# Performance work log

Measured on AMD Instinct MI355X. Metric: run time of the kernel, lower is better.

Reference implementation:

```python
import jax, jax.numpy as jnp
import numpy as np

B, S, D = 2, 2048, 1024
H, DH = 16, 64
DM = 4096
NEG = 1e10


def setup_inputs() -> dict:
    key = jax.random.key(0)
    ks = jax.random.split(key, 8)
    sc = 1.0 / np.sqrt(D)
    return {
        "x": jax.random.normal(ks[0], (B, S, D), jnp.float32),
        "W_Q": jax.random.normal(ks[1], (H, DH, D), jnp.float32) * sc,
        "W_K": jax.random.normal(ks[2], (H, DH, D), jnp.float32) * sc,
        "W_V": jax.random.normal(ks[3], (H, DH, D), jnp.float32) * sc,
        "W_O": jax.random.normal(ks[4], (D, H * DH), jnp.float32) * sc,
        "W_in": jax.random.normal(ks[5], (DM, D), jnp.float32) * sc,
        "b_in": jnp.zeros((DM,), jnp.float32),
        "W_out": jax.random.normal(ks[6], (D, DM), jnp.float32) * sc,
        "b_out": jnp.zeros((D,), jnp.float32),
    }


def reference(x, W_Q, W_K, W_V, W_O, W_in, b_in, W_out, b_out):
    b, s, d = x.shape
    d_head = W_Q.shape[1]
    # --- Attention (faithful to original einsum/mask formulation) ---
    q = jnp.einsum('ihd,bpd->biph', W_Q, x)
    k = jnp.einsum('ihd,bpd->biph', W_K, x)
    v = jnp.einsum('ihd,bpd->biph', W_V, x)
    scores = jnp.einsum('biph,biqh->biqp', k, q)  # [b,i,q,p]
    # original: t.tril(scores) - 1e10 * (1 - triu(ones)) ; mask buffer is triu
    triu = jnp.triu(jnp.ones((s, s), x.dtype))
    masked = jnp.tril(scores) - NEG * (1.0 - triu)
    attn = jax.nn.softmax(masked / np.sqrt(d_head), axis=-1)
    z = jnp.einsum('biph,biqp->biqh', v, attn)          # [b,i,q,h]
    z_flat = z.transpose(0, 2, 1, 3).reshape(b, s, -1)   # b q (i h)
    attn_out = jnp.einsum('df,bqf->bqd', W_O, z_flat)
    # --- Block residual structure (as written: x = attn(x); x = x + x) ---
    mid = attn_out + attn_out
    # --- MLP ---
    pre = jnp.einsum('md,bpd->bpm', W_in, mid) + b_in
    h = jax.nn.relu(pre)
    mlp_out = jnp.einsum('dm,bpm->bpd', W_out, h) + b_out
    return mid + mlp_out
```

## Files before the change

kernel.cpp:

```cpp
#include <hip/hip_runtime.h>
#include <hip/hip_bf16.h>
#include <stdint.h>

typedef unsigned short ushort_t;
typedef __attribute__((ext_vector_type(8))) short short8;
typedef __attribute__((ext_vector_type(4))) float floatx4;

#define DEV __device__ __forceinline__

DEV ushort_t f2b(float f) {
  uint32_t x = __float_as_uint(f);
  uint32_t r = (x + 0x7FFFu + ((x >> 16) & 1u)) >> 16;
  return (ushort_t)r;
}
DEV float b2f(ushort_t u) { return __uint_as_float(((uint32_t)u) << 16); }

DEV void async16(const ushort_t* g, ushort_t* l) {
  __builtin_amdgcn_global_load_lds(
      (const __attribute__((address_space(1))) void*)g,
      (__attribute__((address_space(3))) void*)l, 16, 0, 0);
}

struct Cvt7 {
  const float* src[7];
  ushort_t* dst[7];
  float scale[7];
  unsigned start[8];
};
__global__ void cvt_all(Cvt7 a) {
  unsigned idx = blockIdx.x * blockDim.x + threadIdx.x;
  if (idx >= a.start[7]) return;
  int seg = 0;
#pragma unroll
  for (int j = 1; j < 7; j++) seg += (idx >= a.start[j]) ? 1 : 0;
  unsigned off = idx - a.start[seg];
  float sc = a.scale[seg];
  float4 v = ((const float4*)a.src[seg])[off];
  ((ushort4*)a.dst[seg])[off] =
      make_ushort4(f2b(v.x * sc), f2b(v.y * sc), f2b(v.z * sc), f2b(v.w * sc));
}

template <int MODE, int MT, int SWZ>
__launch_bounds__(256)
__global__ void gemm_bt(const ushort_t* __restrict__ A, const ushort_t* __restrict__ Bm,
                        int M, int N, int Kd, int ldk,
                        ushort_t* __restrict__ outB, float* __restrict__ outF,
                        const float* __restrict__ bias) {
  constexpr int TM = 32 * MT;
  __shared__ alignas(16) ushort_t As[TM * 64];
  __shared__ alignas(16) ushort_t Bs[128 * 64];
  const int tid = threadIdx.x;
  const int wave = tid >> 6, lane = tid & 63;
  const int wm = wave >> 1, wn = wave & 1;

  int bx, by;
  if constexpr (SWZ == 1) {
    const int f = blockIdx.x + gridDim.x * blockIdx.y;
    by = (f & 7) + 8 * (f / (8 * gridDim.x));
    bx = (f >> 3) % gridDim.x;
  } else if constexpr (SWZ == 2) {
    const int x = blockIdx.x, y = blockIdx.y;
    bx = 2 * (x & 3) + (y & 1);
    by = (y >> 1) + 32 * (x >> 2);
  } else {
    bx = blockIdx.x; by = blockIdx.y;
  }
  const int m0 = by * TM, n0 = bx * 128;
  const int kz = blockIdx.z * Kd;

  floatx4 acc[MT][4];
#pragma unroll
  for (int i = 0; i < MT; i++)
#pragma unroll
    for (int j = 0; j < 4; j++) acc[i][j] = (floatx4){0.f, 0.f, 0.f, 0.f};

  const int r8 = lane >> 3;
  const int scol = (((lane & 7) ^ (r8 & 7)) * 8);
  const ushort_t* gA = A + (size_t)(m0 + wave * (TM / 4) + r8) * ldk + kz + scol;
  const ushort_t* gB = Bm + (size_t)(n0 + wave * 32 + r8) * ldk + kz + scol;
  ushort_t* lA = As + wave * (TM / 4) * 64;
  ushort_t* lB = Bs + wave * 2048;

  const int fr = lane & 15, fq = lane >> 4;
  const int sw = fr & 7;
  const ushort_t* rdA = As + (wm * 16 * MT + fr) * 64;
  const ushort_t* rdB = Bs + (wn * 64 + fr) * 64;

  for (int k0 = 0; k0 < Kd; k0 += 64) {
#pragma unroll
    for (int j = 0; j < MT; j++) async16(gA + (size_t)j * 8 * ldk, lA + j * 512);
#pragma unroll
    for (int j = 0; j < 4; j++) async16(gB + (size_t)j * 8 * ldk, lB + j * 512);
    gA += 64; gB += 64;
    __syncthreads();
#pragma unroll
    for (int h = 0; h < 2; h++) {
      const int co = ((h * 4 + fq) ^ sw) * 8;
      short8 af[MT], bfv[4];
#pragma unroll
      for (int mt = 0; mt < MT; mt++) af[mt] = *(const short8*)(rdA + mt * 16 * 64 + co);
#pragma unroll
      for (int nt = 0; nt < 4; nt++) bfv[nt] = *(const short8*)(rdB + nt * 16 * 64 + co);
#pragma unroll
      for (int mt = 0; mt < MT; mt++)
#pragma unroll
        for (int nt = 0; nt < 4; nt++)
          acc[mt][nt] = __builtin_amdgcn_mfma_f32_16x16x32_bf16(af[mt], bfv[nt], acc[mt][nt], 0, 0, 0);
    }
    __syncthreads();
  }

  const int crow = m0 + wm * 16 * MT + (lane >> 4) * 4;
  const int ccol = n0 + wn * 64 + (lane & 15);
  const size_t zoff = (size_t)blockIdx.z * M * N;
#pragma unroll
  for (int mt = 0; mt < MT; mt++)
#pragma unroll
    for (int nt = 0; nt < 4; nt++) {
      floatx4 a = acc[mt][nt];
#pragma unroll
      for (int r = 0; r < 4; r++) {
        const int gm = crow + mt * 16 + r;
        const int gn = ccol + nt * 16;
        const size_t idx = (size_t)gm * N + gn;
        float v = a[r];
        if constexpr (MODE == 0) {
          outB[idx] = f2b(v);
        } else if constexpr (MODE == 1) {
          outB[idx] = f2b(v);
          outF[idx] = v + bias[gn];
        } else if constexpr (MODE == 2) {
          float t = v + bias[gn];
          outB[idx] = f2b(t > 0.f ? t : 0.f);
        } else {
          outF[zoff + idx] = v;
        }
      }
    }
}

template <int MODE>
__launch_bounds__(512, 2)
__global__ void gemm256(const ushort_t* __restrict__ A, const ushort_t* __restrict__ Bm,
                        int M, int N, int Kd, int ldk,
                        ushort_t* __restrict__ outB, float* __restrict__ outF,
                        const float* __restrict__ bias) {
  __shared__ alignas(16) ushort_t As[4][256 * 32];
  __shared__ alignas(16) ushort_t Bs[4][256 * 32];
  const int tid = threadIdx.x;
  const int lane = tid & 63;
  const int wave = tid >> 6;
  const int wm = wave >> 2, wn = wave & 3;

  const int gy = gridDim.y;
  int f = blockIdx.x + gridDim.x * blockIdx.y;
  {
    const int nwg = gridDim.x * gy;
    const int q = nwg >> 3, rr = nwg & 7;
    const int xcd = f & 7, ix = f >> 3;
    f = (xcd < rr ? xcd * (q + 1) : rr * (q + 1) + (xcd - rr) * q) + ix;
  }
  const int bx = f / gy, by = f - gy * bx;
  const int m0 = by * 256, n0 = bx * 256;
  const size_t kz = (size_t)blockIdx.z * Kd;

  floatx4 acc[8][4];
#pragma unroll
  for (int i = 0; i < 8; i++)
#pragma unroll
    for (int j = 0; j < 4; j++) acc[i][j] = (floatx4){0.f, 0.f, 0.f, 0.f};

  const int rloc = tid >> 2, cch = tid & 3;
  const int gcol = ((cch ^ ((rloc >> 1) & 3)) * 8);
  const ushort_t* gA = A + (size_t)(m0 + rloc) * ldk + kz + gcol;
  const ushort_t* gB = Bm + (size_t)(n0 + rloc) * ldk + kz + gcol;
  const int lofs = rloc * 32 + cch * 8;

#define STGA32(bufi, kofs)                                              \
  {                                                                     \
    async16(gA + (kofs), &As[bufi][lofs]);                              \
    async16(gA + (size_t)128 * ldk + (kofs), &As[bufi][4096 + lofs]);   \
  }
#define STGB32(bufi, kofs)                                              \
  {                                                                     \
    async16(gB + (kofs), &Bs[bufi][lofs]);                              \
    async16(gB + (size_t)128 * ldk + (kofs), &Bs[bufi][4096 + lofs]);   \
  }

  const int NT = Kd >> 5;
  STGA32(0, 0) STGB32(0, 0)
  if (NT > 1) { STGA32(1, 32) STGB32(1, 32) }
  if (NT > 2) { STGA32(2, 64) STGB32(2, 64) }
  if (NT > 2) asm volatile("s_waitcnt vmcnt(8)" ::: "memory");
  else if (NT > 1) asm volatile("s_waitcnt vmcnt(4)" ::: "memory");
  else asm volatile("s_waitcnt vmcnt(0)" ::: "memory");
  __builtin_amdgcn_s_barrier();

  const int fr = lane & 15, fq = lane >> 4;
  const int co = ((fq ^ ((fr >> 1) & 3)) * 8);
  const int aoff = (wm * 128 + fr) * 32 + co;
  const int boff = (wn * 64 + fr) * 32 + co;

  for (int kt = 0; kt < NT; ++kt) {
    const int cb = kt & 3;
    const int pb = (kt + 3) & 3;
    const int kof = (kt + 3) * 32;
    const bool sp = (kt + 3) < NT;
    const ushort_t* Ab = As[cb];
    const ushort_t* Bb = Bs[cb];
    short8 av[4], bv[4];

#pragma unroll
    for (int i = 0; i < 4; i++) av[i] = *(const short8*)(Ab + aoff + i * 512);
#pragma unroll
    for (int j = 0; j < 4; j++) bv[j] = *(const short8*)(Bb + boff + j * 512);
    if (sp) STGA32(pb, kof)
    __builtin_amdgcn_s_barrier();
    asm volatile("s_waitcnt lgkmcnt(0)" ::: "memory");
    __builtin_amdgcn_s_setprio(1);
#pragma unroll
    for (int i = 0; i < 4; i++)
#pragma unroll
      for (int j = 0; j < 4; j++)
        acc[i][j] = __builtin_amdgcn_mfma_f32_16x16x32_bf16(av[i], bv[j], acc[i][j], 0, 0, 0);
    __builtin_amdgcn_s_setprio(0);
    __builtin_amdgcn_s_barrier();

#pragma unroll
    for (int i = 0; i < 4; i++) av[i] = *(const short8*)(Ab + aoff + 2048 + i * 512);
    if (sp) STGB32(pb, kof)
    __builtin_amdgcn_s_barrier();
    asm volatile("s_waitcnt lgkmcnt(0)" ::: "memory");
    __builtin_amdgcn_s_setprio(1);
#pragma unroll
    for (int i = 0; i < 4; i++)
#pragma unroll
      for (int j = 0; j < 4; j++)
        acc[4 + i][j] = __builtin_amdgcn_mfma_f32_16x16x32_bf16(av[i], bv[j], acc[4 + i][j], 0, 0, 0);
    __builtin_amdgcn_s_setprio(0);
    if (kt + 3 < NT) asm volatile("s_waitcnt vmcnt(8)" ::: "memory");
    else if (kt + 2 < NT) asm volatile("s_waitcnt vmcnt(4)" ::: "memory");
    else asm volatile("s_waitcnt vmcnt(0)" ::: "memory");
    __builtin_amdgcn_s_barrier();
  }
#undef STGA32
#undef STGB32

  const int crow = m0 + wm * 128 + (lane >> 4) * 4;
  const int ccol = n0 + wn * 64 + (lane & 15);
  const size_t zoff = (size_t)blockIdx.z * ((size_t)M * (size_t)N);
#pragma unroll
  for (int mt = 0; mt < 8; mt++)
#pragma unroll
    for (int nt = 0; nt < 4; nt++) {
      floatx4 a = acc[mt][nt];
#pragma unroll
      for (int r = 0; r < 4; r++) {
        const int gm = crow + mt * 16 + r;
        const int gn = ccol + nt * 16;
        const size_t idx = (size_t)gm * N + gn;
        if constexpr (MODE == 0) {
          outB[idx] = f2b(a[r]);
        } else if constexpr (MODE == 2) {
          float t = a[r] + bias[gn];
          outB[idx] = f2b(t > 0.f ? t : 0.f);
        } else {
          outF[zoff + idx] = a[r];
        }
      }
    }
}

__launch_bounds__(256)
__global__ void reduce4(const float4* __restrict__ P, float4* __restrict__ out, int n4) {
  int i = blockIdx.x * blockDim.x + threadIdx.x;
  int st = gridDim.x * blockDim.x;
  for (; i < n4; i += st) {
    float4 a = out[i];
    float4 p0 = P[i], p1 = P[i + 1048576], p2 = P[i + 2097152], p3 = P[i + 3145728];
    a.x += (p0.x + p1.x) + (p2.x + p3.x);
    a.y += (p0.y + p1.y) + (p2.y + p3.y);
    a.z += (p0.z + p1.z) + (p2.z + p3.z);
    a.w += (p0.w + p1.w) + (p2.w + p3.w);
    out[i] = a;
  }
}

__launch_bounds__(256)
__global__ void attn1(const ushort_t* __restrict__ qkv,
                      float* __restrict__ eG, float* __restrict__ psumG) {
  const int c = blockIdx.x & 63;
  const int i = (blockIdx.x >> 6) & 15;
  const int b = blockIdx.x >> 10;
  const int t = threadIdx.x, wave = t >> 6, h = t & 63;
  const size_t rowbase = (size_t)b * 2048 * 3072;
  float vacc = 0.f;
#pragma unroll
  for (int r = 0; r < 8; r++) {
    const int s = c * 32 + wave * 8 + r;
    const size_t rb = rowbase + (size_t)s * 3072 + i * 64 + h;
    float q = b2f(qkv[rb]);
    float k = b2f(qkv[rb + 1024]);
    float v = b2f(qkv[rb + 2048]);
    float d = q * k;
#pragma unroll
    for (int off = 32; off > 0; off >>= 1) d += __shfl_xor(d, off, 64);
    if (h == 0) eG[((size_t)(b * 16 + i)) * 2048 + s] = __expf(d * 0.125f);
    vacc += v;
  }
  __shared__ float vs[4][64];
  vs[wave][h] = vacc;
  __syncthreads();
  if (t < 64)
    psumG[(((size_t)(b * 16 + i)) * 64 + c) * 64 + t] =
        vs[0][t] + vs[1][t] + vs[2][t] + vs[3][t];
}

__launch_bounds__(256)
__global__ void attn2(const ushort_t* __restrict__ qkv,
                      const float* __restrict__ eG, const float* __restrict__ psumG,
                      ushort_t* __restrict__ Z) {
  const int wave = threadIdx.x >> 6, h = threadIdx.x & 63;
  const int c = (blockIdx.x & 15) * 4 + wave;
  const int i = (blockIdx.x >> 4) & 15;
  const int b = blockIdx.x >> 8;
  const size_t rowbase = (size_t)b * 2048 * 3072;
  const size_t pbase = ((size_t)(b * 16 + i)) * 64;
  float run = 0.f;
#pragma unroll 8
  for (int cc = c + 1; cc < 64; cc++) run += psumG[(pbase + cc) * 64 + h];
  const size_t ebase = ((size_t)(b * 16 + i)) * 2048;
  for (int t4 = 1; t4 >= 0; t4--) {
    float vv[16], ee[16];
#pragma unroll
    for (int j = 0; j < 16; j++) {
      const int s = c * 32 + t4 * 16 + j;
      vv[j] = b2f(qkv[rowbase + (size_t)s * 3072 + 2048 + i * 64 + h]);
      ee[j] = eG[ebase + s];
    }
#pragma unroll
    for (int j = 15; j >= 0; j--) {
      const int s = c * 32 + t4 * 16 + j;
      float z = (ee[j] * vv[j] + run) / (ee[j] + (float)(2047 - s));
      Z[((size_t)b * 2048 + s) * 1024 + i * 64 + h] = f2b(z);
      run += vv[j];
    }
  }
}

extern "C" void kernel_launch(void* const* d_in, const int* in_sizes, int n_in,
                              void* d_out, int out_size, void* d_ws, size_t ws_size,
                              hipStream_t stream) {
  const float* x     = (const float*)d_in[0];
  const float* W_Q   = (const float*)d_in[1];
  const float* W_K   = (const float*)d_in[2];
  const float* W_V   = (const float*)d_in[3];
  const float* W_O   = (const float*)d_in[4];
  const float* W_in  = (const float*)d_in[5];
  const float* b_in  = (const float*)d_in[6];
  const float* W_out = (const float*)d_in[7];
  const float* b_out = (const float*)d_in[8];
  float* out = (float*)d_out;

  char* base = (char*)d_ws;
  const size_t MB = 1048576;
  ushort_t* Xb    = (ushort_t*)(base + 0 * MB);
  ushort_t* Wqkv  = (ushort_t*)(base + 8 * MB);
  ushort_t* WOb   = (ushort_t*)(base + 14 * MB);
  ushort_t* Z     = (ushort_t*)(base + 16 * MB);
  ushort_t* QKV   = (ushort_t*)(base + 24 * MB);
  ushort_t* midb  = (ushort_t*)(base + 48 * MB);
  ushort_t* Winb  = (ushort_t*)(base + 56 * MB);
  ushort_t* Woutb = (ushort_t*)(base + 64 * MB);
  ushort_t* Hb    = (ushort_t*)(base + 72 * MB);
  float*    P     = (float*)(base + 0 * MB);
  float*    psumG = (float*)(base + 72 * MB);
  float*    eG    = (float*)(base + 72 * MB + 524288);

  Cvt7 ca;
  ca.src[0] = x;     ca.dst[0] = Xb;               ca.scale[0] = 1.f;
  ca.src[1] = W_Q;   ca.dst[1] = Wqkv;             ca.scale[1] = 1.f;
  ca.src[2] = W_K;   ca.dst[2] = Wqkv + 1048576;   ca.scale[2] = 1.f;
  ca.src[3] = W_V;   ca.dst[3] = Wqkv + 2097152;   ca.scale[3] = 1.f;
  ca.src[4] = W_O;   ca.dst[4] = WOb;              ca.scale[4] = 2.f;
  ca.src[5] = W_in;  ca.dst[5] = Winb;             ca.scale[5] = 1.f;
  ca.src[6] = W_out; ca.dst[6] = Woutb;            ca.scale[6] = 1.f;
  unsigned n4s[7] = {1048576, 262144, 262144, 262144, 262144, 1048576, 1048576};
  unsigned acc4 = 0;
  for (int j = 0; j < 7; j++) { ca.start[j] = acc4; acc4 += n4s[j]; }
  ca.start[7] = acc4;
  cvt_all<<<dim3((acc4 + 255) / 256), dim3(256), 0, stream>>>(ca);

  gemm256<0><<<dim3(12, 16), 512, 0, stream>>>(Xb, Wqkv, 4096, 3072, 1024, 1024,
                                               QKV, nullptr, nullptr);
  attn1<<<dim3(2048), 256, 0, stream>>>(QKV, eG, psumG);
  attn2<<<dim3(512), 256, 0, stream>>>(QKV, eG, psumG, Z);
  gemm_bt<1, 2, 1><<<dim3(8, 64), 256, 0, stream>>>(Z, WOb, 4096, 1024, 1024, 1024,
                                                    midb, out, b_out);
  gemm256<2><<<dim3(16, 16), 512, 0, stream>>>(midb, Winb, 4096, 4096, 1024, 1024,
                                               Hb, nullptr, b_in);
  gemm256<3><<<dim3(4, 16, 4), 512, 0, stream>>>(Hb, Woutb, 4096, 1024, 1024, 4096,
                                                 nullptr, P, nullptr);
  reduce4<<<dim3(1024), 256, 0, stream>>>((const float4*)P, (float4*)out, 1048576);
}
```

Before: 290.3 us.

## Software-pipeline LDS fragment loads with MFMA in GEMM main loop

Restructures the GEMM K-loop so LDS reads for the next half-tile and the next k-step's A/B fragments are issued before or during the current MFMA block, using double-buffered A registers and interleaving B reloads between MFMA columns. The explicit lgkmcnt waits and one of the two barriers per half are removed, and sched_barrier plus compiler fences pin the ordering. The prologue drops the NT>1/NT>2 guards, assuming K is at least 96. The aim is to hide LDS latency behind matrix instructions and cut barrier stalls, at the cost of more live vector registers and a possible occupancy drop or spills.

```diff
diff --git a/kernel.cpp b/kernel.cpp
--- a/kernel.cpp
+++ b/kernel.cpp
@@ -20,6 +20,8 @@
       (const __attribute__((address_space(1))) void*)g,
       (__attribute__((address_space(3))) void*)l, 16, 0, 0);
 }
+
+#define CFENCE() asm volatile("" ::: "memory")
 
 struct Cvt7 {
   const float* src[7];
@@ -189,59 +191,65 @@
 
   const int NT = Kd >> 5;
   STGA32(0, 0) STGB32(0, 0)
-  if (NT > 1) { STGA32(1, 32) STGB32(1, 32) }
-  if (NT > 2) { STGA32(2, 64) STGB32(2, 64) }
-  if (NT > 2) asm volatile("s_waitcnt vmcnt(8)" ::: "memory");
-  else if (NT > 1) asm volatile("s_waitcnt vmcnt(4)" ::: "memory");
-  else asm volatile("s_waitcnt vmcnt(0)" ::: "memory");
+  STGA32(1, 32) STGB32(1, 32)
+  STGA32(2, 64) STGB32(2, 64)
+  asm volatile("s_waitcnt vmcnt(8)" ::: "memory");
   __builtin_amdgcn_s_barrier();
+  CFENCE();
 
   const int fr = lane & 15, fq = lane >> 4;
   const int co = ((fq ^ ((fr >> 1) & 3)) * 8);
   const int aoff = (wm * 128 + fr) * 32 + co;
   const int boff = (wn * 64 + fr) * 32 + co;
 
+  short8 av0[4], av1[4], bv[4];
+#pragma unroll
+  for (int i = 0; i < 4; i++) av0[i] = *(const short8*)(&As[0][0] + aoff + i * 512);
+#pragma unroll
+  for (int j = 0; j < 4; j++) bv[j] = *(const short8*)(&Bs[0][0] + boff + j * 512);
+
   for (int kt = 0; kt < NT; ++kt) {
     const int cb = kt & 3;
+    const int nb = (kt + 1) & 3;
     const int pb = (kt + 3) & 3;
     const int kof = (kt + 3) * 32;
-    const bool sp = (kt + 3) < NT;
-    const ushort_t* Ab = As[cb];
-    const ushort_t* Bb = Bs[cb];
-    short8 av[4], bv[4];
-
-#pragma unroll
-    for (int i = 0; i < 4; i++) av[i] = *(const short8*)(Ab + aoff + i * 512);
-#pragma unroll
-    for (int j = 0; j < 4; j++) bv[j] = *(const short8*)(Bb + boff + j * 512);
-    if (sp) STGA32(pb, kof)
+    const ushort_t* Ab = &As[cb][0];
+    const ushort_t* An = &As[nb][0];
+    const ushort_t* Bn = &Bs[nb][0];
+
+#pragma unroll
+    for (int i = 0; i < 4; i++) av1[i] = *(const short8*)(Ab + aoff + 2048 + i * 512);
+    if (kt + 3 < NT) STGA32(pb, kof)
+    __builtin_amdgcn_sched_barrier(0);
+    __builtin_amdgcn_s_setprio(1);
+#pragma unroll
+    for (int i = 0; i < 4; i++)
+#pragma unroll
+      for (int j = 0; j < 4; j++)
+        acc[i][j] = __builtin_amdgcn_mfma_f32_16x16x32_bf16(av0[i], bv[j], acc[i][j], 0, 0, 0);
+    __builtin_amdgcn_s_setprio(0);
+    if (kt + 3 < NT)      asm volatile("s_waitcnt vmcnt(6)" ::: "memory");
+    else if (kt + 2 < NT) asm volatile("s_waitcnt vmcnt(4)" ::: "memory");
+    else                  asm volatile("s_waitcnt vmcnt(0)" ::: "memory");
     __builtin_amdgcn_s_barrier();
-    asm volatile("s_waitcnt lgkmcnt(0)" ::: "memory");
+    CFENCE();
+
+#pragma unroll
+    for (int i = 0; i < 4; i++) av0[i] = *(const short8*)(An + aoff + i * 512);
+    if (kt + 3 < NT) STGB32(pb, kof)
+    __builtin_amdgcn_sched_barrier(0);
     __builtin_amdgcn_s_setprio(1);
 #pragma unroll
-    for (int i = 0; i < 4; i++)
-#pragma unroll
-      for (int j = 0; j < 4; j++)
-        acc[i][j] = __builtin_amdgcn_mfma_f32_16x16x32_bf16(av[i], bv[j], acc[i][j], 0, 0, 0);
+    for (int j = 0; j < 4; j++) {
+#pragma unroll
+      for (int i = 0; i < 4; i++)
+        acc[4 + i][j] = __builtin_amdgcn_mfma_f32_16x16x32_bf16(av1[i], bv[j], acc[4 + i][j], 0, 0, 0);
+      bv[j] = *(const short8*)(Bn + boff + j * 512);
+    }
     __builtin_amdgcn_s_setprio(0);
+    CFENCE();
     __builtin_amdgcn_s_barrier();
-
-#pragma unroll
-    for (int i = 0; i < 4; i++) av[i] = *(const short8*)(Ab + aoff + 2048 + i * 512);
-    if (sp) STGB32(pb, kof)
-    __builtin_amdgcn_s_barrier();
-    asm volatile("s_waitcnt lgkmcnt(0)" ::: "memory");
-    __builtin_amdgcn_s_setprio(1);
-#pragma unroll
-    for (int i = 0; i < 4; i++)
-#pragma unroll
-      for (int j = 0; j < 4; j++)
-        acc[4 + i][j] = __builtin_amdgcn_mfma_f32_16x16x32_bf16(av[i], bv[j], acc[4 + i][j], 0, 0, 0);
-    __builtin_amdgcn_s_setprio(0);
-    if (kt + 3 < NT) asm volatile("s_waitcnt vmcnt(8)" ::: "memory");
-    else if (kt + 2 < NT) asm volatile("s_waitcnt vmcnt(4)" ::: "memory");
-    else asm volatile("s_waitcnt vmcnt(0)" ::: "memory");
-    __builtin_amdgcn_s_barrier();
+    CFENCE();
   }
 #undef STGA32
 #undef STGB32
```

After: 292.8 us. No clear change (+0.9%).
